# Optimization experiments

Hardware: AMD Instinct MI355X
Metric: run time of the kernel (lower is better)

The kernel has to match this reference:

```python
import jax, jax.numpy as jnp
import numpy as np

NA_CUTOFF = 30.0
OTHER_CUTOFF = 15.0
THRESHOLDS = jnp.array([0.5, 1.0, 2.0, 4.0], dtype=jnp.float32)


def _cdist(x):
    # x: [b, n, 3] -> [b, n, n] euclidean distances, safe-sqrt (0 grad at 0)
    diff = x[:, :, None, :] - x[:, None, :, :]
    sq = jnp.sum(diff * diff, axis=-1)
    safe = jnp.where(sq > 0, sq, 1.0)
    return jnp.where(sq > 0, jnp.sqrt(safe), 0.0)


def setup_inputs() -> dict:
    key = jax.random.key(0)
    k1, k2, k3, k4, k5 = jax.random.split(key, 5)
    b, n = 2, 4096
    # angstrom-scale coordinates so cutoffs (15/30 A) are meaningful
    true_coords = jax.random.normal(k1, (b, n, 3), dtype=jnp.float32) * 20.0
    pred_coords = true_coords + jax.random.normal(k2, (b, n, 3), dtype=jnp.float32) * 1.0
    is_dna = jax.random.randint(k3, (b, n), 0, 2) > 0
    is_rna = jax.random.randint(k4, (b, n), 0, 2) > 0
    coords_mask = jax.random.randint(k5, (b, n), 0, 2) > 0
    return {
        'pred_coords': pred_coords,
        'true_coords': true_coords,
        'is_dna': is_dna,
        'is_rna': is_rna,
        'coords_mask': coords_mask,
    }


def reference(pred_coords, true_coords, is_dna, is_rna, coords_mask):
    b, n, _ = pred_coords.shape
    pred_dists = _cdist(pred_coords)            # [b, n, n]
    true_dists = _cdist(true_coords)            # [b, n, n]
    dist_diff = jnp.abs(true_dists - pred_dists)
    # eps: sigmoid(threshold - |d_true - d_pred|), averaged over 4 thresholds
    eps = jax.nn.sigmoid(THRESHOLDS - dist_diff[..., None]).mean(axis=-1)  # [b, n, n]

    is_nt = is_dna | is_rna
    nt_pair = is_nt[:, :, None] & is_nt[:, None, :]
    inclusion = jnp.where(nt_pair, true_dists < NA_CUTOFF, true_dists < OTHER_CUTOFF)
    mask = inclusion & ~jnp.eye(n, dtype=bool)[None]
    mask = mask & (coords_mask[:, :, None] & coords_mask[:, None, :])

    maskf = mask.astype(eps.dtype)
    num = (eps * maskf).sum(axis=(-1, -2))
    den = jnp.maximum(maskf.sum(axis=(-1, -2)), 1.0)
    lddt = num / den
    return 1.0 - lddt.mean()
```

## Files before the change

kernel.cpp:

```cpp
#include <hip/hip_runtime.h>
#include <math.h>

#define NTHREADS 256
#define CAP 4096
#define NSBLK 544

#define LUTN 3072
#define OCT_LO (-16)
#define U_MIN 1.52587890625e-5f
#define U_MAX 255.999f
#define IDX_BYTE_BIAS 56832u

typedef float v2f __attribute__((ext_vector_type(2)));

__device__ __forceinline__ float fsqrt(float x) {
#if __has_builtin(__builtin_amdgcn_sqrtf)
    return __builtin_amdgcn_sqrtf(x);
#else
    return sqrtf(x);
#endif
}
__device__ __forceinline__ float fmed3(float x, float lo, float hi) {
#if __has_builtin(__builtin_amdgcn_fmed3f)
    return __builtin_amdgcn_fmed3f(x, lo, hi);
#else
    return fminf(fmaxf(x, lo), hi);
#endif
}

__device__ __forceinline__ float sig4(float d) {
    const float e = expf(d);
    return 1.0f / (1.0f + e * 0.60653065971263342360f)
         + 1.0f / (1.0f + e * 0.36787944117144232160f)
         + 1.0f / (1.0f + e * 0.13533528323661269189f)
         + 1.0f / (1.0f + e * 0.01831563888873418029f);
}

__global__ __launch_bounds__(256) void prep_kernel(
    float* __restrict__ gLUT, float* __restrict__ C, int* __restrict__ Mcnt, int S)
{
    const int gid = blockIdx.x * 256 + threadIdx.x;
    if (gid < LUTN) {
        const int oct = gid >> 7;
        const int k   = gid & 127;
        const float base2 = exp2f((float)(oct + OCT_LO));
        const float umid = base2 * (1.0f + ((float)k + 0.5f) * 0.0078125f);
        gLUT[gid] = sig4(fsqrt(umid));
    }
    if (gid < 2) Mcnt[gid] = 0;
    const int total = 9 * S;
    const int stride = gridDim.x * 256;
    for (int idx = gid; idx < total; idx += stride)
        C[idx] = (idx < 6 * S) ? 1.0e9f : 0.0f;
}

__global__ __launch_bounds__(256) void compact_kernel(
    const float* __restrict__ pred, const float* __restrict__ tru,
    const int* __restrict__ dna, const int* __restrict__ rna,
    const int* __restrict__ cm,
    float* __restrict__ C, int* __restrict__ Mcnt, int n, int S)
{
    __shared__ int scan[256];
    __shared__ int sbase;
    const int chunks = n / 256;
    const int b = blockIdx.x / chunks;
    const int chunk = blockIdx.x % chunks;
    const int tid = threadIdx.x;
    const size_t gi = (size_t)b * n + chunk * 256 + tid;

    const int f = (cm[gi] != 0) ? 1 : 0;
    scan[tid] = f;
    __syncthreads();
    #pragma unroll
    for (int off = 1; off < 256; off <<= 1) {
        const int v = scan[tid];
        const int u = (tid >= off) ? scan[tid - off] : 0;
        __syncthreads();
        scan[tid] = v + u;
        __syncthreads();
    }
    if (tid == 255) sbase = atomicAdd(&Mcnt[b], scan[255]);
    __syncthreads();

    if (f) {
        const int pos = sbase + scan[tid] - 1;
        const float* p = pred + gi * 3;
        const float* q = tru  + gi * 3;
        const int nt = (dna[gi] != 0) || (rna[gi] != 0);
        const int bo = b * CAP;
        C[0 * S + bo + pos] = p[0];  C[1 * S + bo + pos] = p[1];
        C[2 * S + bo + pos] = p[2];  C[3 * S + bo + pos] = q[0];
        C[4 * S + bo + pos] = q[1];  C[5 * S + bo + pos] = q[2];
        C[6 * S + bo + pos] = nt ? 900.0f : 225.0f;
        C[7 * S + bo + pos] = 225.0f;
        C[8 * S + bo + pos] = nt ? 1.0f : 0.0f;
    }
}

__device__ __forceinline__ void pair_tail(float sqp, float sqt, float cut2,
                                          const char* __restrict__ lutB,
                                          float& num, float& den) {
    const float r  = fsqrt(sqt * sqp);
    const float u0 = fmaf(-2.0f, r, sqt + sqp);
    const float u  = fmed3(u0, U_MIN, U_MAX);
    const unsigned int bits = __float_as_uint(u);
    const float s  = *(const float*)(lutB + ((bits >> 14) & ~3u));
    const float m  = (sqt < cut2) ? 1.0f : 0.0f;
    num = fmaf(m, s, num);
    den += m;
}

__global__ __launch_bounds__(NTHREADS) void lddt_tile_kernel(
    const float* __restrict__ C, const int* __restrict__ Mptr,
    const float* __restrict__ gLUT,
    float* __restrict__ pnum, float* __restrict__ pden, int S)
{
    __shared__ __align__(16) float sPX[256], sPY[256], sPZ[256];
    __shared__ __align__(16) float sTX[256], sTY[256], sTZ[256];
    __shared__ __align__(16) float sCut[2 * 256];
    __shared__ __align__(16) float sLUT[LUTN];
    __shared__ float wnum[4], wden[4];

    const int tid = threadIdx.x;

    int s = blockIdx.x;
    const int bi = s / NSBLK;
    s -= bi * NSBLK;
    const int q = s >> 2;
    const int r = s & 3;
    const int W = 33;
    int g = (int)(((float)W - fsqrt((float)(W * W - 8 * q))) * 0.5f);
    while ((g + 1) * 16 - ((g + 1) * g) / 2 <= q) ++g;
    while (g * 16 - (g * (g - 1)) / 2 > q) --g;
    const int sc = g + (q - (g * 16 - (g * (g - 1)) / 2));
    const int ti = 4 * g + r;
    const int i0 = 64 * ti;
    const int J0 = 256 * sc;
    const bool has_diag = (sc == g);
    const int M = Mptr[bi];

    if (i0 >= M || J0 >= M) {
        if (tid == 0) { pnum[blockIdx.x] = 0.0f; pden[blockIdx.x] = 0.0f; }
        return;
    }

    const int bo = bi * CAP;
    const float* cpx = C + 0 * S + bo;  const float* cpy = C + 1 * S + bo;
    const float* cpz = C + 2 * S + bo;  const float* ctx = C + 3 * S + bo;
    const float* cty = C + 4 * S + bo;  const float* ctz = C + 5 * S + bo;
    const float* ccn = C + 6 * S + bo;  const float* cco = C + 7 * S + bo;
    const float* cntf = C + 8 * S + bo;

    {
        const float4* gl4 = (const float4*)gLUT;
        float4* sl4 = (float4*)sLUT;
        #pragma unroll
        for (int e = tid; e < LUTN / 4; e += NTHREADS) sl4[e] = gl4[e];
    }
    {
        const int j = J0 + tid;
        sPX[tid] = cpx[j]; sPY[tid] = cpy[j]; sPZ[tid] = cpz[j];
        sTX[tid] = ctx[j]; sTY[tid] = cty[j]; sTZ[tid] = ctz[j];
        sCut[tid] = ccn[j]; sCut[256 + tid] = cco[j];
    }

    const int w = tid >> 6;
    const int l = tid & 63;
    const int i = i0 + l;
    const float pix = cpx[i], piy = cpy[i], piz = cpz[i];
    const float tix = ctx[i], tiy = cty[i], tiz = ctz[i];
    const bool nti = (cntf[i] != 0.0f);
    __syncthreads();

    const float* cutsel = nti ? &sCut[0] : &sCut[256];
    const char* lutB = (const char*)sLUT - IDX_BYTE_BIAS;
    const int kbase = 16 * w;

    const v2f px2 = {pix, pix}, py2 = {piy, piy}, pz2 = {piz, piz};
    const v2f tx2 = {tix, tix}, ty2 = {tiy, tiy}, tz2 = {tiz, tiz};

    float accn = 0.0f, accd = 0.0f;

    #pragma unroll
    for (int c = 0; c < 4; ++c) {
        const int tj = 4 * sc + c;
        if (tj < ti || 64 * tj >= M) continue;
        const bool diag = has_diag && (c == r);
        const int o = 64 * c;

        float num = 0.0f, den = 0.0f;
        #pragma unroll
        for (int qd = 0; qd < 4; ++qd) {
            const int jq = o + kbase + 4 * qd;
            const float4 PX = *(const float4*)&sPX[jq];
            const float4 PY = *(const float4*)&sPY[jq];
            const float4 PZ = *(const float4*)&sPZ[jq];
            const float4 TX = *(const float4*)&sTX[jq];
            const float4 TY = *(const float4*)&sTY[jq];
            const float4 TZ = *(const float4*)&sTZ[jq];
            const float4 CTC = *(const float4*)&cutsel[jq];

            v2f dx, dy, dz, sqpA, sqpB, sqtA, sqtB;

            dx = px2 - (v2f){PX.x, PX.y}; dy = py2 - (v2f){PY.x, PY.y}; dz = pz2 - (v2f){PZ.x, PZ.y};
            sqpA = dx * dx + dy * dy + dz * dz;
            dx = tx2 - (v2f){TX.x, TX.y}; dy = ty2 - (v2f){TY.x, TY.y}; dz = tz2 - (v2f){TZ.x, TZ.y};
            sqtA = dx * dx + dy * dy + dz * dz;

            dx = px2 - (v2f){PX.z, PX.w}; dy = py2 - (v2f){PY.z, PY.w}; dz = pz2 - (v2f){PZ.z, PZ.w};
            sqpB = dx * dx + dy * dy + dz * dz;
            dx = tx2 - (v2f){TX.z, TX.w}; dy = ty2 - (v2f){TY.z, TY.w}; dz = tz2 - (v2f){TZ.z, TZ.w};
            sqtB = dx * dx + dy * dy + dz * dz;

            pair_tail(sqpA.x, sqtA.x, CTC.x, lutB, num, den);
            pair_tail(sqpA.y, sqtA.y, CTC.y, lutB, num, den);
            pair_tail(sqpB.x, sqtB.x, CTC.z, lutB, num, den);
            pair_tail(sqpB.y, sqtB.y, CTC.w, lutB, num, den);
        }
        const float sc2 = diag ? 1.0f : 2.0f;
        accn = fmaf(sc2, num, accn);
        accd = fmaf(sc2, den, accd);
    }

    if (has_diag && ((l >> 4) == w) && i < M) {
        accn -= sLUT[0];
        accd -= 1.0f;
    }

    #pragma unroll
    for (int off = 32; off > 0; off >>= 1) {
        accn += __shfl_down(accn, off, 64);
        accd += __shfl_down(accd, off, 64);
    }
    if ((tid & 63) == 0) { wnum[w] = accn; wden[w] = accd; }
    __syncthreads();

    if (tid == 0) {
        pnum[blockIdx.x] = wnum[0] + wnum[1] + wnum[2] + wnum[3];
        pden[blockIdx.x] = wden[0] + wden[1] + wden[2] + wden[3];
    }
}

__global__ __launch_bounds__(256) void lddt_final_kernel(
    const float* __restrict__ pnum, const float* __restrict__ pden,
    float* __restrict__ out, int nsblk)
{
    __shared__ double sn0[4], sn1[4], sd0[4], sd1[4];
    double n0 = 0, n1 = 0, d0 = 0, d1 = 0;
    for (int s = threadIdx.x; s < 2 * nsblk; s += 256) {
        if (s < nsblk) { n0 += (double)pnum[s]; d0 += (double)pden[s]; }
        else           { n1 += (double)pnum[s]; d1 += (double)pden[s]; }
    }
    #pragma unroll
    for (int off = 32; off > 0; off >>= 1) {
        n0 += __shfl_down(n0, off, 64); d0 += __shfl_down(d0, off, 64);
        n1 += __shfl_down(n1, off, 64); d1 += __shfl_down(d1, off, 64);
    }
    const int w = threadIdx.x >> 6;
    if ((threadIdx.x & 63) == 0) { sn0[w] = n0; sn1[w] = n1; sd0[w] = d0; sd1[w] = d1; }
    __syncthreads();
    if (threadIdx.x == 0) {
        double N0 = sn0[0] + sn0[1] + sn0[2] + sn0[3];
        double N1 = sn1[0] + sn1[1] + sn1[2] + sn1[3];
        double D0 = sd0[0] + sd0[1] + sd0[2] + sd0[3];
        double D1 = sd1[0] + sd1[1] + sd1[2] + sd1[3];
        D0 = D0 > 1.0 ? D0 : 1.0;
        D1 = D1 > 1.0 ? D1 : 1.0;
        const double l0 = 0.25 * N0 / D0;
        const double l1 = 0.25 * N1 / D1;
        out[0] = (float)(1.0 - 0.5 * (l0 + l1));
    }
}

extern "C" void kernel_launch(void* const* d_in, const int* in_sizes, int n_in,
                              void* d_out, int out_size, void* d_ws, size_t ws_size,
                              hipStream_t stream) {
    const float* pred = (const float*)d_in[0];
    const float* tru  = (const float*)d_in[1];
    const int*   dna  = (const int*)d_in[2];
    const int*   rna  = (const int*)d_in[3];
    const int*   cm   = (const int*)d_in[4];
    float* out = (float*)d_out;

    const int B = 2;
    const int n = in_sizes[2] / B;
    const int S = B * CAP;

    char* p = (char*)d_ws;
    float* gLUT = (float*)p;                 p += (size_t)LUTN * sizeof(float);
    float* C    = (float*)p;                 p += (size_t)9 * S * sizeof(float);
    float* pnum = (float*)p;                 p += (size_t)B * NSBLK * sizeof(float);
    float* pden = (float*)p;                 p += (size_t)B * NSBLK * sizeof(float);
    int*   Mcnt = (int*)p;

    hipLaunchKernelGGL(prep_kernel, dim3(288), dim3(256), 0, stream,
                       gLUT, C, Mcnt, S);
    hipLaunchKernelGGL(compact_kernel, dim3(B * (n / 256)), dim3(256), 0, stream,
                       pred, tru, dna, rna, cm, C, Mcnt, n, S);
    hipLaunchKernelGGL(lddt_tile_kernel, dim3(B * NSBLK), dim3(NTHREADS), 0, stream,
                       C, Mcnt, gLUT, pnum, pden, S);
    hipLaunchKernelGGL(lddt_final_kernel, dim3(1), dim3(256), 0, stream,
                       pnum, pden, out, NSBLK);
}
```

Baseline: 76.76 us.

## Fuse prep into compact and final reduction into tile kernel via atomics

Removes the separate prep kernel by building the LUT inside compact_kernel. The padding of C with sentinel values is replaced by explicit j<M and i<M validity masking. The separate final reduction kernel is removed: each tile block atomically adds its partial sums into double accumulators, and the last block, identified by an atomic ticket, computes the output. This cuts two launches and replaces them with a memset, at the cost of global atomics and possible reads of stale padding coordinates.

```diff
diff --git a/kernel.cpp b/kernel.cpp
--- a/kernel.cpp
+++ b/kernel.cpp
@@ -36,10 +36,18 @@
          + 1.0f / (1.0f + e * 0.01831563888873418029f);
 }
 
-__global__ __launch_bounds__(256) void prep_kernel(
-    float* __restrict__ gLUT, float* __restrict__ C, int* __restrict__ Mcnt, int S)
+__global__ __launch_bounds__(256) void compact_kernel(
+    const float* __restrict__ pred, const float* __restrict__ tru,
+    const int* __restrict__ dna, const int* __restrict__ rna,
+    const int* __restrict__ cm,
+    float* __restrict__ C, float* __restrict__ gLUT,
+    int* __restrict__ Mcnt, int n, int S)
 {
-    const int gid = blockIdx.x * 256 + threadIdx.x;
+    __shared__ int scan[256];
+    __shared__ int sbase;
+    const int tid = threadIdx.x;
+    const int gid = blockIdx.x * 256 + tid;
+
     if (gid < LUTN) {
         const int oct = gid >> 7;
         const int k   = gid & 127;
@@ -47,25 +55,10 @@
         const float umid = base2 * (1.0f + ((float)k + 0.5f) * 0.0078125f);
         gLUT[gid] = sig4(fsqrt(umid));
     }
-    if (gid < 2) Mcnt[gid] = 0;
-    const int total = 9 * S;
-    const int stride = gridDim.x * 256;
-    for (int idx = gid; idx < total; idx += stride)
-        C[idx] = (idx < 6 * S) ? 1.0e9f : 0.0f;
-}
-
-__global__ __launch_bounds__(256) void compact_kernel(
-    const float* __restrict__ pred, const float* __restrict__ tru,
-    const int* __restrict__ dna, const int* __restrict__ rna,
-    const int* __restrict__ cm,
-    float* __restrict__ C, int* __restrict__ Mcnt, int n, int S)
-{
-    __shared__ int scan[256];
-    __shared__ int sbase;
+
     const int chunks = n / 256;
     const int b = blockIdx.x / chunks;
     const int chunk = blockIdx.x % chunks;
-    const int tid = threadIdx.x;
     const size_t gi = (size_t)b * n + chunk * 256 + tid;
 
     const int f = (cm[gi] != 0) ? 1 : 0;
@@ -113,7 +106,8 @@
 __global__ __launch_bounds__(NTHREADS) void lddt_tile_kernel(
     const float* __restrict__ C, const int* __restrict__ Mptr,
     const float* __restrict__ gLUT,
-    float* __restrict__ pnum, float* __restrict__ pden, int S)
+    double* __restrict__ gnum, double* __restrict__ gden,
+    int* __restrict__ ticket, float* __restrict__ out, int S, int nblk_total)
 {
     __shared__ __align__(16) float sPX[256], sPY[256], sPZ[256];
     __shared__ __align__(16) float sTX[256], sTY[256], sTZ[256];
@@ -139,136 +133,127 @@
     const bool has_diag = (sc == g);
     const int M = Mptr[bi];
 
-    if (i0 >= M || J0 >= M) {
-        if (tid == 0) { pnum[blockIdx.x] = 0.0f; pden[blockIdx.x] = 0.0f; }
-        return;
-    }
-
-    const int bo = bi * CAP;
-    const float* cpx = C + 0 * S + bo;  const float* cpy = C + 1 * S + bo;
-    const float* cpz = C + 2 * S + bo;  const float* ctx = C + 3 * S + bo;
-    const float* cty = C + 4 * S + bo;  const float* ctz = C + 5 * S + bo;
-    const float* ccn = C + 6 * S + bo;  const float* cco = C + 7 * S + bo;
-    const float* cntf = C + 8 * S + bo;
-
-    {
-        const float4* gl4 = (const float4*)gLUT;
-        float4* sl4 = (float4*)sLUT;
+    float tn = 0.0f, td = 0.0f;
+    if (i0 < M && J0 < M) {
+        const int bo = bi * CAP;
+        const float* cpx = C + 0 * S + bo;  const float* cpy = C + 1 * S + bo;
+        const float* cpz = C + 2 * S + bo;  const float* ctx = C + 3 * S + bo;
+        const float* cty = C + 4 * S + bo;  const float* ctz = C + 5 * S + bo;
+        const float* ccn = C + 6 * S + bo;  const float* cco = C + 7 * S + bo;
+        const float* cntf = C + 8 * S + bo;
+
+        {
+            const float4* gl4 = (const float4*)gLUT;
+            float4* sl4 = (float4*)sLUT;
+            #pragma unroll
+            for (int e = tid; e < LUTN / 4; e += NTHREADS) sl4[e] = gl4[e];
+        }
+        {
+            const int j = J0 + tid;
+            const bool jv = (j < M);
+            sPX[tid] = cpx[j]; sPY[tid] = cpy[j]; sPZ[tid] = cpz[j];
+            sTX[tid] = ctx[j]; sTY[tid] = cty[j]; sTZ[tid] = ctz[j];
+            sCut[tid]       = jv ? ccn[j] : 0.0f;
+            sCut[256 + tid] = jv ? cco[j] : 0.0f;
+        }
+
+        const int w = tid >> 6;
+        const int l = tid & 63;
+        const int i = i0 + l;
+        const float pix = cpx[i], piy = cpy[i], piz = cpz[i];
+        const float tix = ctx[i], tiy = cty[i], tiz = ctz[i];
+        const bool nti = (cntf[i] != 0.0f);
+        const float valid = (i < M) ? 1.0f : 0.0f;
+        __syncthreads();
+
+        const float* cutsel = nti ? &sCut[0] : &sCut[256];
+        const char* lutB = (const char*)sLUT - IDX_BYTE_BIAS;
+        const int kbase = 16 * w;
+
+        const v2f px2 = {pix, pix}, py2 = {piy, piy}, pz2 = {piz, piz};
+        const v2f tx2 = {tix, tix}, ty2 = {tiy, tiy}, tz2 = {tiz, tiz};
+
+        float accn = 0.0f, accd = 0.0f;
+
         #pragma unroll
-        for (int e = tid; e < LUTN / 4; e += NTHREADS) sl4[e] = gl4[e];
-    }
-    {
-        const int j = J0 + tid;
-        sPX[tid] = cpx[j]; sPY[tid] = cpy[j]; sPZ[tid] = cpz[j];
-        sTX[tid] = ctx[j]; sTY[tid] = cty[j]; sTZ[tid] = ctz[j];
-        sCut[tid] = ccn[j]; sCut[256 + tid] = cco[j];
-    }
-
-    const int w = tid >> 6;
-    const int l = tid & 63;
-    const int i = i0 + l;
-    const float pix = cpx[i], piy = cpy[i], piz = cpz[i];
-    const float tix = ctx[i], tiy = cty[i], tiz = ctz[i];
-    const bool nti = (cntf[i] != 0.0f);
-    __syncthreads();
-
-    const float* cutsel = nti ? &sCut[0] : &sCut[256];
-    const char* lutB = (const char*)sLUT - IDX_BYTE_BIAS;
-    const int kbase = 16 * w;
-
-    const v2f px2 = {pix, pix}, py2 = {piy, piy}, pz2 = {piz, piz};
-    const v2f tx2 = {tix, tix}, ty2 = {tiy, tiy}, tz2 = {tiz, tiz};
-
-    float accn = 0.0f, accd = 0.0f;
-
-    #pragma unroll
-    for (int c = 0; c < 4; ++c) {
-        const int tj = 4 * sc + c;
-        if (tj < ti || 64 * tj >= M) continue;
-        const bool diag = has_diag && (c == r);
-        const int o = 64 * c;
-
-        float num = 0.0f, den = 0.0f;
+        for (int c = 0; c < 4; ++c) {
+            const int tj = 4 * sc + c;
+            if (tj < ti || 64 * tj >= M) continue;
+            const bool diag = has_diag && (c == r);
+            const int o = 64 * c;
+
+            float num = 0.0f, den = 0.0f;
+            #pragma unroll
+            for (int qd = 0; qd < 4; ++qd) {
+                const int jq = o + kbase + 4 * qd;
+                const float4 PX = *(const float4*)&sPX[jq];
+                const float4 PY = *(const float4*)&sPY[jq];
+                const float4 PZ = *(const float4*)&sPZ[jq];
+                const float4 TX = *(const float4*)&sTX[jq];
+                const float4 TY = *(const float4*)&sTY[jq];
+                const float4 TZ = *(const float4*)&sTZ[jq];
+                const float4 CTC = *(const float4*)&cutsel[jq];
+
+                v2f dx, dy, dz, sqpA, sqpB, sqtA, sqtB;
+
+                dx = px2 - (v2f){PX.x, PX.y}; dy = py2 - (v2f){PY.x, PY.y}; dz = pz2 - (v2f){PZ.x, PZ.y};
+                sqpA = dx * dx + dy * dy + dz * dz;
+                dx = tx2 - (v2f){TX.x, TX.y}; dy = ty2 - (v2f){TY.x, TY.y}; dz = tz2 - (v2f){TZ.x, TZ.y};
+                sqtA = dx * dx + dy * dy + dz * dz;
+
+                dx = px2 - (v2f){PX.z, PX.w}; dy = py2 - (v2f){PY.z, PY.w}; dz = pz2 - (v2f){PZ.z, PZ.w};
+                sqpB = dx * dx + dy * dy + dz * dz;
+                dx = tx2 - (v2f){TX.z, TX.w}; dy = ty2 - (v2f){TY.z, TY.w}; dz = tz2 - (v2f){TZ.z, TZ.w};
+                sqtB = dx * dx + dy * dy + dz * dz;
+
+                pair_tail(sqpA.x, sqtA.x, CTC.x, lutB, num, den);
+                pair_tail(sqpA.y, sqtA.y, CTC.y, lutB, num, den);
+                pair_tail(sqpB.x, sqtB.x, CTC.z, lutB, num, den);
+                pair_tail(sqpB.y, sqtB.y, CTC.w, lutB, num, den);
+            }
+            const float sc2 = diag ? 1.0f : 2.0f;
+            accn = fmaf(sc2, num, accn);
+            accd = fmaf(sc2, den, accd);
+        }
+
+        accn *= valid;
+        accd *= valid;
+        if (has_diag && ((l >> 4) == w) && i < M) {
+            accn -= sLUT[0];
+            accd -= 1.0f;
+        }
+
         #pragma unroll
-        for (int qd = 0; qd < 4; ++qd) {
-            const int jq = o + kbase + 4 * qd;
-            const float4 PX = *(const float4*)&sPX[jq];
-            const float4 PY = *(const float4*)&sPY[jq];
-            const float4 PZ = *(const float4*)&sPZ[jq];
-            const float4 TX = *(const float4*)&sTX[jq];
-            const float4 TY = *(const float4*)&sTY[jq];
-            const float4 TZ = *(const float4*)&sTZ[jq];
-            const float4 CTC = *(const float4*)&cutsel[jq];
-
-            v2f dx, dy, dz, sqpA, sqpB, sqtA, sqtB;
-
-            dx = px2 - (v2f){PX.x, PX.y}; dy = py2 - (v2f){PY.x, PY.y}; dz = pz2 - (v2f){PZ.x, PZ.y};
-            sqpA = dx * dx + dy * dy + dz * dz;
-            dx = tx2 - (v2f){TX.x, TX.y}; dy = ty2 - (v2f){TY.x, TY.y}; dz = tz2 - (v2f){TZ.x, TZ.y};
-            sqtA = dx * dx + dy * dy + dz * dz;
-
-            dx = px2 - (v2f){PX.z, PX.w}; dy = py2 - (v2f){PY.z, PY.w}; dz = pz2 - (v2f){PZ.z, PZ.w};
-            sqpB = dx * dx + dy * dy + dz * dz;
-            dx = tx2 - (v2f){TX.z, TX.w}; dy = ty2 - (v2f){TY.z, TY.w}; dz = tz2 - (v2f){TZ.z, TZ.w};
-            sqtB = dx * dx + dy * dy + dz * dz;
-
-            pair_tail(sqpA.x, sqtA.x, CTC.x, lutB, num, den);
-            pair_tail(sqpA.y, sqtA.y, CTC.y, lutB, num, den);
-            pair_tail(sqpB.x, sqtB.x, CTC.z, lutB, num, den);
-            pair_tail(sqpB.y, sqtB.y, CTC.w, lutB, num, den);
-        }
-        const float sc2 = diag ? 1.0f : 2.0f;
-        accn = fmaf(sc2, num, accn);
-        accd = fmaf(sc2, den, accd);
-    }
-
-    if (has_diag && ((l >> 4) == w) && i < M) {
-        accn -= sLUT[0];
-        accd -= 1.0f;
-    }
-
-    #pragma unroll
-    for (int off = 32; off > 0; off >>= 1) {
-        accn += __shfl_down(accn, off, 64);
-        accd += __shfl_down(accd, off, 64);
-    }
-    if ((tid & 63) == 0) { wnum[w] = accn; wden[w] = accd; }
-    __syncthreads();
+        for (int off = 32; off > 0; off >>= 1) {
+            accn += __shfl_down(accn, off, 64);
+            accd += __shfl_down(accd, off, 64);
+        }
+        if ((tid & 63) == 0) { wnum[w] = accn; wden[w] = accd; }
+        __syncthreads();
+        if (tid == 0) {
+            tn = wnum[0] + wnum[1] + wnum[2] + wnum[3];
+            td = wden[0] + wden[1] + wden[2] + wden[3];
+        }
+    }
 
     if (tid == 0) {
-        pnum[blockIdx.x] = wnum[0] + wnum[1] + wnum[2] + wnum[3];
-        pden[blockIdx.x] = wden[0] + wden[1] + wden[2] + wden[3];
-    }
-}
-
-__global__ __launch_bounds__(256) void lddt_final_kernel(
-    const float* __restrict__ pnum, const float* __restrict__ pden,
-    float* __restrict__ out, int nsblk)
-{
-    __shared__ double sn0[4], sn1[4], sd0[4], sd1[4];
-    double n0 = 0, n1 = 0, d0 = 0, d1 = 0;
-    for (int s = threadIdx.x; s < 2 * nsblk; s += 256) {
-        if (s < nsblk) { n0 += (double)pnum[s]; d0 += (double)pden[s]; }
-        else           { n1 += (double)pnum[s]; d1 += (double)pden[s]; }
-    }
-    #pragma unroll
-    for (int off = 32; off > 0; off >>= 1) {
-        n0 += __shfl_down(n0, off, 64); d0 += __shfl_down(d0, off, 64);
-        n1 += __shfl_down(n1, off, 64); d1 += __shfl_down(d1, off, 64);
-    }
-    const int w = threadIdx.x >> 6;
-    if ((threadIdx.x & 63) == 0) { sn0[w] = n0; sn1[w] = n1; sd0[w] = d0; sd1[w] = d1; }
-    __syncthreads();
-    if (threadIdx.x == 0) {
-        double N0 = sn0[0] + sn0[1] + sn0[2] + sn0[3];
-        double N1 = sn1[0] + sn1[1] + sn1[2] + sn1[3];
-        double D0 = sd0[0] + sd0[1] + sd0[2] + sd0[3];
-        double D1 = sd1[0] + sd1[1] + sd1[2] + sd1[3];
-        D0 = D0 > 1.0 ? D0 : 1.0;
-        D1 = D1 > 1.0 ? D1 : 1.0;
-        const double l0 = 0.25 * N0 / D0;
-        const double l1 = 0.25 * N1 / D1;
-        out[0] = (float)(1.0 - 0.5 * (l0 + l1));
+        if (tn != 0.0f || td != 0.0f) {
+            atomicAdd(&gnum[bi], (double)tn);
+            atomicAdd(&gden[bi], (double)td);
+        }
+        __threadfence();
+        const int t = atomicAdd(ticket, 1);
+        if (t == nblk_total - 1) {
+            const double N0 = atomicAdd(&gnum[0], 0.0);
+            const double N1 = atomicAdd(&gnum[1], 0.0);
+            double D0 = atomicAdd(&gden[0], 0.0);
+            double D1 = atomicAdd(&gden[1], 0.0);
+            D0 = D0 > 1.0 ? D0 : 1.0;
+            D1 = D1 > 1.0 ? D1 : 1.0;
+            const double l0 = 0.25 * N0 / D0;
+            const double l1 = 0.25 * N1 / D1;
+            out[0] = (float)(1.0 - 0.5 * (l0 + l1));
+        }
     }
 }
 
@@ -289,16 +274,15 @@
     char* p = (char*)d_ws;
     float* gLUT = (float*)p;                 p += (size_t)LUTN * sizeof(float);
     float* C    = (float*)p;                 p += (size_t)9 * S * sizeof(float);
-    float* pnum = (float*)p;                 p += (size_t)B * NSBLK * sizeof(float);
-    float* pden = (float*)p;                 p += (size_t)B * NSBLK * sizeof(float);
-    int*   Mcnt = (int*)p;
-
-    hipLaunchKernelGGL(prep_kernel, dim3(288), dim3(256), 0, stream,
-                       gLUT, C, Mcnt, S);
+    double* gnum = (double*)p;               p += 2 * sizeof(double);
+    double* gden = (double*)p;               p += 2 * sizeof(double);
+    int* Mcnt   = (int*)p;                   p += 2 * sizeof(int);
+    int* ticket = (int*)p;
+
+    hipMemsetAsync(gnum, 0, 48, stream);
+
     hipLaunchKernelGGL(compact_kernel, dim3(B * (n / 256)), dim3(256), 0, stream,
-                       pred, tru, dna, rna, cm, C, Mcnt, n, S);
+                       pred, tru, dna, rna, cm, C, gLUT, Mcnt, n, S);
     hipLaunchKernelGGL(lddt_tile_kernel, dim3(B * NSBLK), dim3(NTHREADS), 0, stream,
-                       C, Mcnt, gLUT, pnum, pden, S);
-    hipLaunchKernelGGL(lddt_final_kernel, dim3(1), dim3(256), 0, stream,
-                       pnum, pden, out, NSBLK);
-}
+                       C, Mcnt, gLUT, gnum, gden, ticket, out, S, B * NSBLK);
+}
```

After: 92.19 us. 1.2x slower.
